# Kernel optimization log

Measured on AMD Instinct MI355X. Metric: run time of the kernel, lower is better.

The kernel has to match this reference:

```python
import jax, jax.numpy as jnp
import numpy as np

D_MODEL = 1024
NUM_HEADS = 16
D_K = D_MODEL // NUM_HEADS
B, S = 2, 2048


def setup_inputs() -> dict:
    key = jax.random.key(0)
    ks = jax.random.split(key, 11)
    scale = 1.0 / np.sqrt(D_MODEL)
    inp = {
        "Q": jax.random.normal(ks[0], (B, S, D_MODEL), jnp.float32),
        "K": jax.random.normal(ks[1], (B, S, D_MODEL), jnp.float32),
        "V": jax.random.normal(ks[2], (B, S, D_MODEL), jnp.float32),
        "mask": jnp.tril(jnp.ones((S, S), jnp.int32))[None, None, :, :],  # causal [1,1,S,S]
        "Wq": jax.random.normal(ks[3], (D_MODEL, D_MODEL), jnp.float32) * scale,
        "bq": jax.random.normal(ks[4], (D_MODEL,), jnp.float32) * scale,
        "Wk": jax.random.normal(ks[5], (D_MODEL, D_MODEL), jnp.float32) * scale,
        "bk": jax.random.normal(ks[6], (D_MODEL,), jnp.float32) * scale,
        "Wv": jax.random.normal(ks[7], (D_MODEL, D_MODEL), jnp.float32) * scale,
        "bv": jax.random.normal(ks[8], (D_MODEL,), jnp.float32) * scale,
        "Wo": jax.random.normal(ks[9], (D_MODEL, D_MODEL), jnp.float32) * scale,
        "bo": jax.random.normal(ks[10], (D_MODEL,), jnp.float32) * scale,
    }
    return inp


def _split_heads(x):
    b, s, _ = x.shape
    return x.reshape(b, s, NUM_HEADS, D_K).transpose(0, 2, 1, 3)  # [B,H,S,d_k]


def reference(Q, K, V, mask, Wq, bq, Wk, bk, Wv, bv, Wo, bo):
    q = _split_heads(Q @ Wq.T + bq)
    k = _split_heads(K @ Wk.T + bk)
    v = _split_heads(V @ Wv.T + bv)
    scores = jnp.einsum("bhqd,bhkd->bhqk", q, k) / jnp.sqrt(jnp.float32(D_K))
    scores = jnp.where(mask == 0, jnp.float32(-1e9), scores)
    probs = jax.nn.softmax(scores, axis=-1)
    attn = jnp.einsum("bhqk,bhkd->bhqd", probs, v)  # [B,H,S,d_k]
    attn = attn.transpose(0, 2, 1, 3).reshape(Q.shape[0], Q.shape[1], D_MODEL)
    return attn @ Wo.T + bo
```

## Files before the change

### kernel.cpp

```cpp
#include <hip/hip_runtime.h>
#include <hip/hip_bf16.h>

typedef __attribute__((ext_vector_type(8))) short short8;
typedef __attribute__((ext_vector_type(4))) short short4v;
typedef __attribute__((ext_vector_type(4))) float f32x4;
typedef __attribute__((ext_vector_type(4))) int i32x4;

static __device__ __forceinline__ short f2bf(float f) {
    __hip_bfloat16 h = __float2bfloat16(f);
    return __builtin_bit_cast(short, h);
}

static __device__ __forceinline__ float exp2fast(float x) {
    float r;
    asm("v_exp_f32 %0, %1" : "=v"(r) : "v"(x));
    return r;
}

static __device__ __forceinline__ unsigned cvt_pk_bf16(float a, float b) {
    unsigned r;
    asm("v_cvt_pk_bf16_f32 %0, %1, %2" : "=v"(r) : "v"(a), "v"(b));
    return r;
}

#define GLOAD16(g, l) __builtin_amdgcn_global_load_lds( \
    (const __attribute__((address_space(1))) void*)(g), \
    (__attribute__((address_space(3))) void*)(l), 16, 0, 0)

__global__ __launch_bounds__(256) void convert_all(
        const float* __restrict__ q, const float* __restrict__ k, const float* __restrict__ v,
        const float* __restrict__ wq, const float* __restrict__ wk,
        const float* __restrict__ wv, const float* __restrict__ wo,
        short* __restrict__ oq, short* __restrict__ ok, short* __restrict__ ov,
        short* __restrict__ owq, short* __restrict__ owk,
        short* __restrict__ owv, short* __restrict__ owo) {
    const int y = blockIdx.y;
    const float* in;
    short* out;
    int n4;
    switch (y) {
        case 0: in = q;  out = oq;  n4 = 1048576; break;
        case 1: in = k;  out = ok;  n4 = 1048576; break;
        case 2: in = v;  out = ov;  n4 = 1048576; break;
        case 3: in = wq; out = owq; n4 = 262144;  break;
        case 4: in = wk; out = owk; n4 = 262144;  break;
        case 5: in = wv; out = owv; n4 = 262144;  break;
        default: in = wo; out = owo; n4 = 262144; break;
    }
    int i = blockIdx.x * blockDim.x + threadIdx.x;
    int stride = gridDim.x * blockDim.x;
    for (; i < n4; i += stride) {
        f32x4 vv = reinterpret_cast<const f32x4*>(in)[i];
        short4v o;
        o.x = f2bf(vv.x); o.y = f2bf(vv.y); o.z = f2bf(vv.z); o.w = f2bf(vv.w);
        reinterpret_cast<short4v*>(out)[i] = o;
    }
}

__global__ __launch_bounds__(256, 3) void gemm_qkv(
        const short* __restrict__ Qb, const short* __restrict__ Kb, const short* __restrict__ Vb,
        const short* __restrict__ Wq, const short* __restrict__ Wk, const short* __restrict__ Wv,
        const float* __restrict__ bq, const float* __restrict__ bk, const float* __restrict__ bv,
        short* __restrict__ q_, short* __restrict__ k_, short* __restrict__ vT) {
    __shared__ __align__(16) short aS[128 * 64];
    __shared__ __align__(16) short bS[128 * 64];
    const int tid = threadIdx.x;
    const int lane = tid & 63;
    const int w = tid >> 6;
    const int wr = w >> 1, wc = w & 1;
    const int l15 = lane & 15, lq = lane >> 4;
    const int lr = lane >> 3;
    const int lcs = ((lane & 7) ^ lr) * 8;
    const int y = blockIdx.y;
    const int wg = (blockIdx.x & 7) * 32 + (blockIdx.x >> 3);
    const int bn = wg & 7;
    const int bm = wg >> 3;

    const short* A = y == 0 ? Qb : y == 1 ? Kb : Vb;
    const short* W = y == 0 ? Wq : y == 1 ? Wk : Wv;
    const float* bias = y == 0 ? bq : y == 1 ? bk : bv;
    const short* Ab = A + (size_t)(bm * 128) * 1024;
    const short* Wb = W + (size_t)(bn * 128) * 1024;

    f32x4 acc[4][4] = {};

    for (int t = 0; t < 16; ++t) {
        const int k0 = t * 64;
#pragma unroll
        for (int j = 0; j < 4; ++j) {
            int r0 = w * 32 + j * 8;
            GLOAD16(&Ab[(size_t)(r0 + lr) * 1024 + k0 + lcs], &aS[r0 * 64]);
        }
#pragma unroll
        for (int j = 0; j < 4; ++j) {
            int r0 = w * 32 + j * 8;
            GLOAD16(&Wb[(size_t)(r0 + lr) * 1024 + k0 + lcs], &bS[r0 * 64]);
        }
        asm volatile("s_waitcnt vmcnt(0)" ::: "memory");
        __builtin_amdgcn_s_barrier();
#pragma unroll
        for (int kf = 0; kf < 2; ++kf) {
            const int ck = ((kf * 4 + lq) ^ (l15 & 7)) * 8;
            short8 af[4], bfr[4];
#pragma unroll
            for (int mi = 0; mi < 4; ++mi)
                af[mi] = *reinterpret_cast<const short8*>(
                    &aS[(wr * 64 + mi * 16 + l15) * 64 + ck]);
#pragma unroll
            for (int ni = 0; ni < 4; ++ni)
                bfr[ni] = *reinterpret_cast<const short8*>(
                    &bS[(wc * 64 + ni * 16 + l15) * 64 + ck]);
#pragma unroll
            for (int mi = 0; mi < 4; ++mi)
#pragma unroll
                for (int ni = 0; ni < 4; ++ni)
                    acc[mi][ni] = __builtin_amdgcn_mfma_f32_16x16x32_bf16(
                        af[mi], bfr[ni], acc[mi][ni], 0, 0, 0);
        }
        asm volatile("s_waitcnt lgkmcnt(0)" ::: "memory");
        __builtin_amdgcn_sched_barrier(0);
        __builtin_amdgcn_s_barrier();
    }

    const float QSCALE = 0.125f * 1.44269504f;
#pragma unroll
    for (int mi = 0; mi < 4; ++mi) {
#pragma unroll
        for (int ni = 0; ni < 4; ++ni) {
#pragma unroll
            for (int i = 0; i < 4; ++i) {
                int m = bm * 128 + wr * 64 + mi * 16 + lq * 4 + i;
                int n = bn * 128 + wc * 64 + ni * 16 + l15;
                float v = acc[mi][ni][i] + bias[n];
                int b = m >> 11, s = m & 2047, h = n >> 6, d = n & 63;
                if (y == 0) {
                    q_[((size_t)(b * 16 + h) * 2048 + s) * 64 + d] = f2bf(v * QSCALE);
                } else if (y == 1) {
                    k_[((size_t)(b * 16 + h) * 2048 + s) * 64 + d] = f2bf(v);
                } else {
                    vT[((size_t)(b * 16 + h) * 64 + d) * 2048 + s] = f2bf(v);
                }
            }
        }
    }
}

__device__ __forceinline__ void gemm_kloop(
        const short* __restrict__ Abase, const short* __restrict__ Wbase,
        short* aSb, short* bSb, f32x4 (&acc)[4][2], int w, int lane) {
    const int lr = lane >> 3;
    const int lcs = ((lane & 7) ^ lr) * 8;
    const int l15 = lane & 15, lq = lane >> 4;
    const int wr = w >> 1, wc = w & 1;
    const int cA0 = ((0 + lq) ^ (l15 & 7)) * 8;
    const int cA1 = ((4 + lq) ^ (l15 & 7)) * 8;

#pragma unroll
    for (int j = 0; j < 4; ++j) {
        int r0 = w * 32 + j * 8;
        GLOAD16(&Abase[(size_t)(r0 + lr) * 1024 + lcs], &aSb[r0 * 64]);
    }
#pragma unroll
    for (int j = 0; j < 2; ++j) {
        int r0 = w * 16 + j * 8;
        GLOAD16(&Wbase[(size_t)(r0 + lr) * 1024 + lcs], &bSb[r0 * 64]);
    }

    for (int t = 0; t < 16; ++t) {
        const int cur = t & 1;
        if (t < 15) {
            const int k0 = (t + 1) * 64;
            const int nb = cur ^ 1;
#pragma unroll
            for (int j = 0; j < 4; ++j) {
                int r0 = w * 32 + j * 8;
                GLOAD16(&Abase[(size_t)(r0 + lr) * 1024 + k0 + lcs], &aSb[nb * 8192 + r0 * 64]);
            }
#pragma unroll
            for (int j = 0; j < 2; ++j) {
                int r0 = w * 16 + j * 8;
                GLOAD16(&Wbase[(size_t)(r0 + lr) * 1024 + k0 + lcs], &bSb[nb * 4096 + r0 * 64]);
            }
            asm volatile("s_waitcnt vmcnt(6)" ::: "memory");
        } else {
            asm volatile("s_waitcnt vmcnt(0)" ::: "memory");
        }
        __builtin_amdgcn_s_barrier();
        __builtin_amdgcn_sched_barrier(0);
#pragma unroll
        for (int kf = 0; kf < 2; ++kf) {
            const int ck = kf ? cA1 : cA0;
            short8 af[4], bfr[2];
#pragma unroll
            for (int mi = 0; mi < 4; ++mi)
                af[mi] = *reinterpret_cast<const short8*>(
                    &aSb[cur * 8192 + (wr * 64 + mi * 16 + l15) * 64 + ck]);
#pragma unroll
            for (int ni = 0; ni < 2; ++ni)
                bfr[ni] = *reinterpret_cast<const short8*>(
                    &bSb[cur * 4096 + (wc * 32 + ni * 16 + l15) * 64 + ck]);
#pragma unroll
            for (int mi = 0; mi < 4; ++mi)
#pragma unroll
                for (int ni = 0; ni < 2; ++ni)
                    acc[mi][ni] = __builtin_amdgcn_mfma_f32_16x16x32_bf16(
                        af[mi], bfr[ni], acc[mi][ni], 0, 0, 0);
        }
        asm volatile("s_waitcnt lgkmcnt(0)" ::: "memory");
        __builtin_amdgcn_sched_barrier(0);
        __builtin_amdgcn_s_barrier();
    }
}

__global__ __launch_bounds__(256, 3) void gemm_o(
        const short* __restrict__ A, const short* __restrict__ W,
        const float* __restrict__ bias, float* __restrict__ out) {
    __shared__ __align__(16) short aSb[2 * 128 * 64];
    __shared__ __align__(16) short bSb[2 * 64 * 64];
    const int tid = threadIdx.x;
    const int lane = tid & 63;
    const int w = tid >> 6;
    const int wg = (blockIdx.x & 7) * 64 + (blockIdx.x >> 3);
    const int bn = wg & 15;
    const int bm = wg >> 4;
    const int l15 = lane & 15, lq = lane >> 4;
    const int wr = w >> 1, wc = w & 1;

    f32x4 acc[4][2] = {};
    gemm_kloop(&A[(size_t)(bm * 128) * 1024], &W[(size_t)(bn * 64) * 1024],
               aSb, bSb, acc, w, lane);

#pragma unroll
    for (int mi = 0; mi < 4; ++mi)
#pragma unroll
        for (int ni = 0; ni < 2; ++ni)
#pragma unroll
            for (int i = 0; i < 4; ++i) {
                int m = bm * 128 + wr * 64 + mi * 16 + lq * 4 + i;
                int n = bn * 64 + wc * 32 + ni * 16 + l15;
                out[(size_t)m * 1024 + n] = acc[mi][ni][i] + bias[n];
            }
}

__global__ __launch_bounds__(256, 4) void attn_fwd(
        const short* __restrict__ qh, const short* __restrict__ kh,
        const short* __restrict__ vT, short* __restrict__ attn) {
    __shared__ __align__(16) short kS[64 * 64];
    __shared__ __align__(16) short vS[64 * 64];
    const int tid = threadIdx.x;
    const int lane = tid & 63;
    const int l15 = lane & 15, lq = lane >> 4;
    const int w = tid >> 6;
    const int hi = (lane >> 5) & 1;
    const int bh = blockIdx.x & 31;
    const int qt = 31 - (blockIdx.x >> 5);
    const int b = bh >> 4, h = bh & 15;
    const size_t head = (size_t)bh * 2048 * 64;
    const short* qp = qh + head;
    const short* kp = kh + head;
    const short* vp = vT + head;
    const int qw0 = qt * 64 + w * 16;

    short8 qf_[2];
#pragma unroll
    for (int kf = 0; kf < 2; ++kf)
        qf_[kf] = *reinterpret_cast<const short8*>(
            &qp[(size_t)(qw0 + l15) * 64 + kf * 32 + lq * 8]);

    f32x4 o[4] = {};
    float m_ = -1e30f, l_ = 0.f;

    const int sr = tid >> 3;
    const int sc8 = tid & 7;
    const int scg = sc8 * 8;
    const int sls = sr * 64 + (sc8 ^ (sr & 7)) * 8;
    const int sls2 = (sr + 32) * 64 + (sc8 ^ (sr & 7)) * 8;

    const int nt = qt + 1;
    short8 kra = *reinterpret_cast<const short8*>(&kp[(size_t)sr * 64 + scg]);
    short8 krb = *reinterpret_cast<const short8*>(&kp[(size_t)(sr + 32) * 64 + scg]);
    short8 vra = *reinterpret_cast<const short8*>(&vp[(size_t)sr * 2048 + scg]);
    short8 vrb = *reinterpret_cast<const short8*>(&vp[(size_t)(sr + 32) * 2048 + scg]);
    *reinterpret_cast<short8*>(&kS[sls]) = kra;
    *reinterpret_cast<short8*>(&kS[sls2]) = krb;
    *reinterpret_cast<short8*>(&vS[sls]) = vra;
    *reinterpret_cast<short8*>(&vS[sls2]) = vrb;
    __syncthreads();

    for (int t = 0; t < nt; ++t) {
        if (t + 1 < nt) {
            kra = *reinterpret_cast<const short8*>(
                &kp[(size_t)((t + 1) * 64 + sr) * 64 + scg]);
            krb = *reinterpret_cast<const short8*>(
                &kp[(size_t)((t + 1) * 64 + sr + 32) * 64 + scg]);
            vra = *reinterpret_cast<const short8*>(
                &vp[(size_t)sr * 2048 + (t + 1) * 64 + scg]);
            vrb = *reinterpret_cast<const short8*>(
                &vp[(size_t)(sr + 32) * 2048 + (t + 1) * 64 + scg]);
        }
        f32x4 s[4] = {};
#pragma unroll
        for (int kf = 0; kf < 2; ++kf) {
            short8 kfr[4];
#pragma unroll
            for (int cf = 0; cf < 4; ++cf)
                kfr[cf] = *reinterpret_cast<const short8*>(
                    &kS[(cf * 16 + l15) * 64 + ((kf * 4 + lq) ^ (l15 & 7)) * 8]);
#pragma unroll
            for (int cf = 0; cf < 4; ++cf)
                s[cf] = __builtin_amdgcn_mfma_f32_16x16x32_bf16(
                    kfr[cf], qf_[kf], s[cf], 0, 0, 0);
        }
        if (t == qt) {
            const int q = qw0 + l15;
#pragma unroll
            for (int cf = 0; cf < 4; ++cf)
#pragma unroll
                for (int i = 0; i < 4; ++i)
                    if (t * 64 + cf * 16 + lq * 4 + i > q) s[cf][i] = -1e30f;
        }
        float pmax = fmaxf(fmaxf(fmaxf(s[0][0], s[0][1]), fmaxf(s[0][2], s[0][3])),
                           fmaxf(fmaxf(s[1][0], s[1][1]), fmaxf(s[1][2], s[1][3])));
        pmax = fmaxf(pmax, fmaxf(fmaxf(fmaxf(s[2][0], s[2][1]), fmaxf(s[2][2], s[2][3])),
                                 fmaxf(fmaxf(s[3][0], s[3][1]), fmaxf(s[3][2], s[3][3]))));
        pmax = fmaxf(pmax, __shfl_xor(pmax, 16));
        pmax = fmaxf(pmax, __shfl_xor(pmax, 32));
        if (!__all(pmax - m_ <= 8.0f)) {
            float mnew = fmaxf(m_, pmax);
            float scl = exp2fast(m_ - mnew);
            m_ = mnew;
            l_ *= scl;
            float s0 = __shfl(scl, lq * 4 + 0);
            float s1 = __shfl(scl, lq * 4 + 1);
            float s2 = __shfl(scl, lq * 4 + 2);
            float s3 = __shfl(scl, lq * 4 + 3);
#pragma unroll
            for (int df = 0; df < 4; ++df) {
                o[df][0] *= s0; o[df][1] *= s1; o[df][2] *= s2; o[df][3] *= s3;
            }
        }
        float rsum = 0.f;
        unsigned P8[8];
#pragma unroll
        for (int cf = 0; cf < 4; ++cf) {
            float p0 = exp2fast(s[cf][0] - m_);
            float p1 = exp2fast(s[cf][1] - m_);
            float p2 = exp2fast(s[cf][2] - m_);
            float p3 = exp2fast(s[cf][3] - m_);
            rsum += (p0 + p1) + (p2 + p3);
            P8[2 * cf]     = cvt_pk_bf16(p0, p1);
            P8[2 * cf + 1] = cvt_pk_bf16(p2, p3);
        }
        rsum += __shfl_xor(rsum, 16);
        rsum += __shfl_xor(rsum, 32);
        l_ += rsum;
#pragma unroll
        for (int kk = 0; kk < 2; ++kk) {
            int dw[4];
#pragma unroll
            for (int j = 0; j < 4; ++j) {
                int src = l15 + 16 * (2 * (lq & 1) + (j >> 1));
                int vlo = __shfl((int)P8[4 * kk + (j & 1)], src);
                int vhi = __shfl((int)P8[4 * kk + 2 + (j & 1)], src);
                dw[j] = hi ? vhi : vlo;
            }
            i32x4 dwv; dwv.x = dw[0]; dwv.y = dw[1]; dwv.z = dw[2]; dwv.w = dw[3];
            short8 pa = __builtin_bit_cast(short8, dwv);
            short8 vb[4];
#pragma unroll
            for (int df = 0; df < 4; ++df)
                vb[df] = *reinterpret_cast<const short8*>(
                    &vS[(df * 16 + l15) * 64 + ((kk * 4 + lq) ^ (l15 & 7)) * 8]);
#pragma unroll
            for (int df = 0; df < 4; ++df)
                o[df] = __builtin_amdgcn_mfma_f32_16x16x32_bf16(
                    pa, vb[df], o[df], 0, 0, 0);
        }
        __syncthreads();
        if (t + 1 < nt) {
            *reinterpret_cast<short8*>(&kS[sls]) = kra;
            *reinterpret_cast<short8*>(&kS[sls2]) = krb;
            *reinterpret_cast<short8*>(&vS[sls]) = vra;
            *reinterpret_cast<short8*>(&vS[sls2]) = vrb;
        }
        __syncthreads();
    }

#pragma unroll
    for (int i = 0; i < 4; ++i) {
        float li = __shfl(l_, lq * 4 + i);
        float rinv = 1.0f / li;
        int sg = qw0 + lq * 4 + i;
        size_t mrow = (size_t)b * 2048 + sg;
#pragma unroll
        for (int df = 0; df < 4; ++df) {
            int col = h * 64 + df * 16 + l15;
            attn[mrow * 1024 + col] = f2bf(o[df][i] * rinv);
        }
    }
}

extern "C" void kernel_launch(void* const* d_in, const int* in_sizes, int n_in,
                              void* d_out, int out_size, void* d_ws, size_t ws_size,
                              hipStream_t stream) {
    const float* Q  = (const float*)d_in[0];
    const float* K  = (const float*)d_in[1];
    const float* V  = (const float*)d_in[2];
    const float* Wq = (const float*)d_in[4];
    const float* bq = (const float*)d_in[5];
    const float* Wk = (const float*)d_in[6];
    const float* bk = (const float*)d_in[7];
    const float* Wv = (const float*)d_in[8];
    const float* bv = (const float*)d_in[9];
    const float* Wo = (const float*)d_in[10];
    const float* bo = (const float*)d_in[11];

    char* ws = (char*)d_ws;
    short* Qb   = (short*)(ws);
    short* Kb   = (short*)(ws + 8388608);
    short* Vb   = (short*)(ws + 16777216);
    short* Wqb  = (short*)(ws + 25165824);
    short* Wkb  = (short*)(ws + 27262976);
    short* Wvb  = (short*)(ws + 29360128);
    short* Wob  = (short*)(ws + 31457280);
    short* q_   = (short*)(ws + 33554432);
    short* k_   = (short*)(ws + 41943040);
    short* vT   = (short*)(ws + 50331648);
    short* attn = Qb;

    dim3 cb(256);
    convert_all<<<dim3(512, 7), cb, 0, stream>>>(Q, K, V, Wq, Wk, Wv, Wo,
                                                 Qb, Kb, Vb, Wqb, Wkb, Wvb, Wob);

    gemm_qkv<<<dim3(256, 3), cb, 0, stream>>>(Qb, Kb, Vb, Wqb, Wkb, Wvb,
                                              bq, bk, bv, q_, k_, vT);

    attn_fwd<<<dim3(1024), cb, 0, stream>>>(q_, k_, vT, attn);

    gemm_o<<<dim3(512), cb, 0, stream>>>(attn, Wob, bo, (float*)d_out);
}
```

Before: 222.1 us.

## Pair causal q-tiles per block, stage vT stores via LDS, retile output GEMM

The attention kernel now gives each block two query tiles (p and 31-p), so causal work is balanced and each K/V tile loaded into LDS serves both tiles. The grid shrinks to 512 blocks and the occupancy hint drops to 2. The V projection epilogue transposes through LDS so it can write 16-byte coalesced stores to vT instead of scattered 2-byte ones. The output GEMM moves to 128x128 tiles with a single-buffered k-loop and 256 blocks. That gives fewer blocks per CU and loses the global-load prefetch overlap the old double-buffered loop had.

```diff
diff --git a/kernel.cpp b/kernel.cpp
--- a/kernel.cpp
+++ b/kernel.cpp
@@ -62,8 +62,9 @@
         const short* __restrict__ Wq, const short* __restrict__ Wk, const short* __restrict__ Wv,
         const float* __restrict__ bq, const float* __restrict__ bk, const float* __restrict__ bv,
         short* __restrict__ q_, short* __restrict__ k_, short* __restrict__ vT) {
-    __shared__ __align__(16) short aS[128 * 64];
-    __shared__ __align__(16) short bS[128 * 64];
+    __shared__ __align__(16) short lds[2 * 128 * 64];
+    short* aS = lds;
+    short* bS = lds + 8192;
     const int tid = threadIdx.x;
     const int lane = tid & 63;
     const int w = tid >> 6;
@@ -123,126 +124,129 @@
     }
 
     const float QSCALE = 0.125f * 1.44269504f;
-#pragma unroll
-    for (int mi = 0; mi < 4; ++mi) {
-#pragma unroll
-        for (int ni = 0; ni < 4; ++ni) {
+    if (y < 2) {
+#pragma unroll
+        for (int mi = 0; mi < 4; ++mi) {
+#pragma unroll
+            for (int ni = 0; ni < 4; ++ni) {
+#pragma unroll
+                for (int i = 0; i < 4; ++i) {
+                    int m = bm * 128 + wr * 64 + mi * 16 + lq * 4 + i;
+                    int n = bn * 128 + wc * 64 + ni * 16 + l15;
+                    float v = acc[mi][ni][i] + bias[n];
+                    int b = m >> 11, s = m & 2047, h = n >> 6, d = n & 63;
+                    if (y == 0)
+                        q_[((size_t)(b * 16 + h) * 2048 + s) * 64 + d] = f2bf(v * QSCALE);
+                    else
+                        k_[((size_t)(b * 16 + h) * 2048 + s) * 64 + d] = f2bf(v);
+                }
+            }
+        }
+    } else {
+#pragma unroll
+        for (int mi = 0; mi < 4; ++mi) {
+#pragma unroll
+            for (int ni = 0; ni < 4; ++ni) {
+                int nl = wc * 64 + ni * 16 + l15;
+                int cc = wr * 8 + mi * 2 + (lq >> 1);
+                int addr = nl * 128 + ((cc ^ (nl & 15)) * 8) + (lq & 1) * 4;
+                short4v pk;
+                pk.x = f2bf(acc[mi][ni][0] + bias[bn * 128 + nl]);
+                pk.y = f2bf(acc[mi][ni][1] + bias[bn * 128 + nl]);
+                pk.z = f2bf(acc[mi][ni][2] + bias[bn * 128 + nl]);
+                pk.w = f2bf(acc[mi][ni][3] + bias[bn * 128 + nl]);
+                *reinterpret_cast<short4v*>(&lds[addr]) = pk;
+            }
+        }
+        __syncthreads();
+        const int bb = bm >> 4;
+        const int s0base = (bm & 15) * 128;
+#pragma unroll
+        for (int j = 0; j < 8; ++j) {
+            int rr = w * 32 + (j & 1) * 16 + (lane >> 2);
+            int cc2 = (j >> 1) * 4 + (lane & 3);
+            short8 val = *reinterpret_cast<const short8*>(
+                &lds[rr * 128 + ((cc2 ^ (rr & 15)) * 8)]);
+            int n = bn * 128 + rr;
+            int hh = n >> 6, d = n & 63;
+            *reinterpret_cast<short8*>(
+                &vT[((size_t)(bb * 16 + hh) * 64 + d) * 2048 + s0base + cc2 * 8]) = val;
+        }
+    }
+}
+
+__global__ __launch_bounds__(256, 3) void gemm_o(
+        const short* __restrict__ A, const short* __restrict__ W,
+        const float* __restrict__ bias, float* __restrict__ out) {
+    __shared__ __align__(16) short lds[2 * 128 * 64];
+    short* aS = lds;
+    short* bS = lds + 8192;
+    const int tid = threadIdx.x;
+    const int lane = tid & 63;
+    const int w = tid >> 6;
+    const int wr = w >> 1, wc = w & 1;
+    const int l15 = lane & 15, lq = lane >> 4;
+    const int lr = lane >> 3;
+    const int lcs = ((lane & 7) ^ lr) * 8;
+    const int wg = (blockIdx.x & 7) * 32 + (blockIdx.x >> 3);
+    const int bn = wg & 7;
+    const int bm = wg >> 3;
+    const short* Ab = A + (size_t)(bm * 128) * 1024;
+    const short* Wb = W + (size_t)(bn * 128) * 1024;
+
+    f32x4 acc[4][4] = {};
+
+    for (int t = 0; t < 16; ++t) {
+        const int k0 = t * 64;
+#pragma unroll
+        for (int j = 0; j < 4; ++j) {
+            int r0 = w * 32 + j * 8;
+            GLOAD16(&Ab[(size_t)(r0 + lr) * 1024 + k0 + lcs], &aS[r0 * 64]);
+        }
+#pragma unroll
+        for (int j = 0; j < 4; ++j) {
+            int r0 = w * 32 + j * 8;
+            GLOAD16(&Wb[(size_t)(r0 + lr) * 1024 + k0 + lcs], &bS[r0 * 64]);
+        }
+        asm volatile("s_waitcnt vmcnt(0)" ::: "memory");
+        __builtin_amdgcn_s_barrier();
+#pragma unroll
+        for (int kf = 0; kf < 2; ++kf) {
+            const int ck = ((kf * 4 + lq) ^ (l15 & 7)) * 8;
+            short8 af[4], bfr[4];
+#pragma unroll
+            for (int mi = 0; mi < 4; ++mi)
+                af[mi] = *reinterpret_cast<const short8*>(
+                    &aS[(wr * 64 + mi * 16 + l15) * 64 + ck]);
+#pragma unroll
+            for (int ni = 0; ni < 4; ++ni)
+                bfr[ni] = *reinterpret_cast<const short8*>(
+                    &bS[(wc * 64 + ni * 16 + l15) * 64 + ck]);
+#pragma unroll
+            for (int mi = 0; mi < 4; ++mi)
+#pragma unroll
+                for (int ni = 0; ni < 4; ++ni)
+                    acc[mi][ni] = __builtin_amdgcn_mfma_f32_16x16x32_bf16(
+                        af[mi], bfr[ni], acc[mi][ni], 0, 0, 0);
+        }
+        asm volatile("s_waitcnt lgkmcnt(0)" ::: "memory");
+        __builtin_amdgcn_sched_barrier(0);
+        __builtin_amdgcn_s_barrier();
+    }
+
+#pragma unroll
+    for (int mi = 0; mi < 4; ++mi)
+#pragma unroll
+        for (int ni = 0; ni < 4; ++ni)
 #pragma unroll
             for (int i = 0; i < 4; ++i) {
                 int m = bm * 128 + wr * 64 + mi * 16 + lq * 4 + i;
                 int n = bn * 128 + wc * 64 + ni * 16 + l15;
-                float v = acc[mi][ni][i] + bias[n];
-                int b = m >> 11, s = m & 2047, h = n >> 6, d = n & 63;
-                if (y == 0) {
-                    q_[((size_t)(b * 16 + h) * 2048 + s) * 64 + d] = f2bf(v * QSCALE);
-                } else if (y == 1) {
-                    k_[((size_t)(b * 16 + h) * 2048 + s) * 64 + d] = f2bf(v);
-                } else {
-                    vT[((size_t)(b * 16 + h) * 64 + d) * 2048 + s] = f2bf(v);
-                }
-            }
-        }
-    }
-}
-
-__device__ __forceinline__ void gemm_kloop(
-        const short* __restrict__ Abase, const short* __restrict__ Wbase,
-        short* aSb, short* bSb, f32x4 (&acc)[4][2], int w, int lane) {
-    const int lr = lane >> 3;
-    const int lcs = ((lane & 7) ^ lr) * 8;
-    const int l15 = lane & 15, lq = lane >> 4;
-    const int wr = w >> 1, wc = w & 1;
-    const int cA0 = ((0 + lq) ^ (l15 & 7)) * 8;
-    const int cA1 = ((4 + lq) ^ (l15 & 7)) * 8;
-
-#pragma unroll
-    for (int j = 0; j < 4; ++j) {
-        int r0 = w * 32 + j * 8;
-        GLOAD16(&Abase[(size_t)(r0 + lr) * 1024 + lcs], &aSb[r0 * 64]);
-    }
-#pragma unroll
-    for (int j = 0; j < 2; ++j) {
-        int r0 = w * 16 + j * 8;
-        GLOAD16(&Wbase[(size_t)(r0 + lr) * 1024 + lcs], &bSb[r0 * 64]);
-    }
-
-    for (int t = 0; t < 16; ++t) {
-        const int cur = t & 1;
-        if (t < 15) {
-            const int k0 = (t + 1) * 64;
-            const int nb = cur ^ 1;
-#pragma unroll
-            for (int j = 0; j < 4; ++j) {
-                int r0 = w * 32 + j * 8;
-                GLOAD16(&Abase[(size_t)(r0 + lr) * 1024 + k0 + lcs], &aSb[nb * 8192 + r0 * 64]);
-            }
-#pragma unroll
-            for (int j = 0; j < 2; ++j) {
-                int r0 = w * 16 + j * 8;
-                GLOAD16(&Wbase[(size_t)(r0 + lr) * 1024 + k0 + lcs], &bSb[nb * 4096 + r0 * 64]);
-            }
-            asm volatile("s_waitcnt vmcnt(6)" ::: "memory");
-        } else {
-            asm volatile("s_waitcnt vmcnt(0)" ::: "memory");
-        }
-        __builtin_amdgcn_s_barrier();
-        __builtin_amdgcn_sched_barrier(0);
-#pragma unroll
-        for (int kf = 0; kf < 2; ++kf) {
-            const int ck = kf ? cA1 : cA0;
-            short8 af[4], bfr[2];
-#pragma unroll
-            for (int mi = 0; mi < 4; ++mi)
-                af[mi] = *reinterpret_cast<const short8*>(
-                    &aSb[cur * 8192 + (wr * 64 + mi * 16 + l15) * 64 + ck]);
-#pragma unroll
-            for (int ni = 0; ni < 2; ++ni)
-                bfr[ni] = *reinterpret_cast<const short8*>(
-                    &bSb[cur * 4096 + (wc * 32 + ni * 16 + l15) * 64 + ck]);
-#pragma unroll
-            for (int mi = 0; mi < 4; ++mi)
-#pragma unroll
-                for (int ni = 0; ni < 2; ++ni)
-                    acc[mi][ni] = __builtin_amdgcn_mfma_f32_16x16x32_bf16(
-                        af[mi], bfr[ni], acc[mi][ni], 0, 0, 0);
-        }
-        asm volatile("s_waitcnt lgkmcnt(0)" ::: "memory");
-        __builtin_amdgcn_sched_barrier(0);
-        __builtin_amdgcn_s_barrier();
-    }
-}
-
-__global__ __launch_bounds__(256, 3) void gemm_o(
-        const short* __restrict__ A, const short* __restrict__ W,
-        const float* __restrict__ bias, float* __restrict__ out) {
-    __shared__ __align__(16) short aSb[2 * 128 * 64];
-    __shared__ __align__(16) short bSb[2 * 64 * 64];
-    const int tid = threadIdx.x;
-    const int lane = tid & 63;
-    const int w = tid >> 6;
-    const int wg = (blockIdx.x & 7) * 64 + (blockIdx.x >> 3);
-    const int bn = wg & 15;
-    const int bm = wg >> 4;
-    const int l15 = lane & 15, lq = lane >> 4;
-    const int wr = w >> 1, wc = w & 1;
-
-    f32x4 acc[4][2] = {};
-    gemm_kloop(&A[(size_t)(bm * 128) * 1024], &W[(size_t)(bn * 64) * 1024],
-               aSb, bSb, acc, w, lane);
-
-#pragma unroll
-    for (int mi = 0; mi < 4; ++mi)
-#pragma unroll
-        for (int ni = 0; ni < 2; ++ni)
-#pragma unroll
-            for (int i = 0; i < 4; ++i) {
-                int m = bm * 128 + wr * 64 + mi * 16 + lq * 4 + i;
-                int n = bn * 64 + wc * 32 + ni * 16 + l15;
                 out[(size_t)m * 1024 + n] = acc[mi][ni][i] + bias[n];
             }
 }
 
-__global__ __launch_bounds__(256, 4) void attn_fwd(
+__global__ __launch_bounds__(256, 2) void attn_fwd(
         const short* __restrict__ qh, const short* __restrict__ kh,
         const short* __restrict__ vT, short* __restrict__ attn) {
     __shared__ __align__(16) short kS[64 * 64];
@@ -253,22 +257,27 @@
     const int w = tid >> 6;
     const int hi = (lane >> 5) & 1;
     const int bh = blockIdx.x & 31;
-    const int qt = 31 - (blockIdx.x >> 5);
+    const int p = blockIdx.x >> 5;
+    const int qtL = p, qtH = 31 - p;
     const int b = bh >> 4, h = bh & 15;
     const size_t head = (size_t)bh * 2048 * 64;
     const short* qp = qh + head;
     const short* kp = kh + head;
     const short* vp = vT + head;
-    const int qw0 = qt * 64 + w * 16;
-
-    short8 qf_[2];
-#pragma unroll
-    for (int kf = 0; kf < 2; ++kf)
-        qf_[kf] = *reinterpret_cast<const short8*>(
-            &qp[(size_t)(qw0 + l15) * 64 + kf * 32 + lq * 8]);
-
-    f32x4 o[4] = {};
-    float m_ = -1e30f, l_ = 0.f;
+    const int qL0 = qtL * 64 + w * 16;
+    const int qH0 = qtH * 64 + w * 16;
+
+    short8 qfL_[2], qfH_[2];
+#pragma unroll
+    for (int kf = 0; kf < 2; ++kf) {
+        qfL_[kf] = *reinterpret_cast<const short8*>(
+            &qp[(size_t)(qL0 + l15) * 64 + kf * 32 + lq * 8]);
+        qfH_[kf] = *reinterpret_cast<const short8*>(
+            &qp[(size_t)(qH0 + l15) * 64 + kf * 32 + lq * 8]);
+    }
+
+    f32x4 oH[4] = {}, oL[4] = {};
+    float mH = -1e30f, lH = 0.f, mL = -1e30f, lL = 0.f;
 
     const int sr = tid >> 3;
     const int sc8 = tid & 7;
@@ -276,49 +285,8 @@
     const int sls = sr * 64 + (sc8 ^ (sr & 7)) * 8;
     const int sls2 = (sr + 32) * 64 + (sc8 ^ (sr & 7)) * 8;
 
-    const int nt = qt + 1;
-    short8 kra = *reinterpret_cast<const short8*>(&kp[(size_t)sr * 64 + scg]);
-    short8 krb = *reinterpret_cast<const short8*>(&kp[(size_t)(sr + 32) * 64 + scg]);
-    short8 vra = *reinterpret_cast<const short8*>(&vp[(size_t)sr * 2048 + scg]);
-    short8 vrb = *reinterpret_cast<const short8*>(&vp[(size_t)(sr + 32) * 2048 + scg]);
-    *reinterpret_cast<short8*>(&kS[sls]) = kra;
-    *reinterpret_cast<short8*>(&kS[sls2]) = krb;
-    *reinterpret_cast<short8*>(&vS[sls]) = vra;
-    *reinterpret_cast<short8*>(&vS[sls2]) = vrb;
-    __syncthreads();
-
-    for (int t = 0; t < nt; ++t) {
-        if (t + 1 < nt) {
-            kra = *reinterpret_cast<const short8*>(
-                &kp[(size_t)((t + 1) * 64 + sr) * 64 + scg]);
-            krb = *reinterpret_cast<const short8*>(
-                &kp[(size_t)((t + 1) * 64 + sr + 32) * 64 + scg]);
-            vra = *reinterpret_cast<const short8*>(
-                &vp[(size_t)sr * 2048 + (t + 1) * 64 + scg]);
-            vrb = *reinterpret_cast<const short8*>(
-                &vp[(size_t)(sr + 32) * 2048 + (t + 1) * 64 + scg]);
-        }
-        f32x4 s[4] = {};
-#pragma unroll
-        for (int kf = 0; kf < 2; ++kf) {
-            short8 kfr[4];
-#pragma unroll
-            for (int cf = 0; cf < 4; ++cf)
-                kfr[cf] = *reinterpret_cast<const short8*>(
-                    &kS[(cf * 16 + l15) * 64 + ((kf * 4 + lq) ^ (l15 & 7)) * 8]);
-#pragma unroll
-            for (int cf = 0; cf < 4; ++cf)
-                s[cf] = __builtin_amdgcn_mfma_f32_16x16x32_bf16(
-                    kfr[cf], qf_[kf], s[cf], 0, 0, 0);
-        }
-        if (t == qt) {
-            const int q = qw0 + l15;
-#pragma unroll
-            for (int cf = 0; cf < 4; ++cf)
-#pragma unroll
-                for (int i = 0; i < 4; ++i)
-                    if (t * 64 + cf * 16 + lq * 4 + i > q) s[cf][i] = -1e30f;
-        }
+    auto softmax = [&](f32x4 (&s)[4], float& m_, float& l_, f32x4 (&o)[4],
+                       unsigned (&P8)[8]) {
         float pmax = fmaxf(fmaxf(fmaxf(s[0][0], s[0][1]), fmaxf(s[0][2], s[0][3])),
                            fmaxf(fmaxf(s[1][0], s[1][1]), fmaxf(s[1][2], s[1][3])));
         pmax = fmaxf(pmax, fmaxf(fmaxf(fmaxf(s[2][0], s[2][1]), fmaxf(s[2][2], s[2][3])),
@@ -340,7 +308,6 @@
             }
         }
         float rsum = 0.f;
-        unsigned P8[8];
 #pragma unroll
         for (int cf = 0; cf < 4; ++cf) {
             float p0 = exp2fast(s[cf][0] - m_);
@@ -354,27 +321,108 @@
         rsum += __shfl_xor(rsum, 16);
         rsum += __shfl_xor(rsum, 32);
         l_ += rsum;
+    };
+
+    const int nt = qtH + 1;
+    short8 kra = *reinterpret_cast<const short8*>(&kp[(size_t)sr * 64 + scg]);
+    short8 krb = *reinterpret_cast<const short8*>(&kp[(size_t)(sr + 32) * 64 + scg]);
+    short8 vra = *reinterpret_cast<const short8*>(&vp[(size_t)sr * 2048 + scg]);
+    short8 vrb = *reinterpret_cast<const short8*>(&vp[(size_t)(sr + 32) * 2048 + scg]);
+    *reinterpret_cast<short8*>(&kS[sls]) = kra;
+    *reinterpret_cast<short8*>(&kS[sls2]) = krb;
+    *reinterpret_cast<short8*>(&vS[sls]) = vra;
+    *reinterpret_cast<short8*>(&vS[sls2]) = vrb;
+    __syncthreads();
+
+    for (int t = 0; t < nt; ++t) {
+        if (t + 1 < nt) {
+            kra = *reinterpret_cast<const short8*>(
+                &kp[(size_t)((t + 1) * 64 + sr) * 64 + scg]);
+            krb = *reinterpret_cast<const short8*>(
+                &kp[(size_t)((t + 1) * 64 + sr + 32) * 64 + scg]);
+            vra = *reinterpret_cast<const short8*>(
+                &vp[(size_t)sr * 2048 + (t + 1) * 64 + scg]);
+            vrb = *reinterpret_cast<const short8*>(
+                &vp[(size_t)(sr + 32) * 2048 + (t + 1) * 64 + scg]);
+        }
+        const bool la = (t <= qtL);
+        f32x4 sH[4] = {}, sL[4] = {};
+#pragma unroll
+        for (int kf = 0; kf < 2; ++kf) {
+            short8 kfr[4];
+#pragma unroll
+            for (int cf = 0; cf < 4; ++cf)
+                kfr[cf] = *reinterpret_cast<const short8*>(
+                    &kS[(cf * 16 + l15) * 64 + ((kf * 4 + lq) ^ (l15 & 7)) * 8]);
+#pragma unroll
+            for (int cf = 0; cf < 4; ++cf)
+                sH[cf] = __builtin_amdgcn_mfma_f32_16x16x32_bf16(
+                    kfr[cf], qfH_[kf], sH[cf], 0, 0, 0);
+            if (la) {
+#pragma unroll
+                for (int cf = 0; cf < 4; ++cf)
+                    sL[cf] = __builtin_amdgcn_mfma_f32_16x16x32_bf16(
+                        kfr[cf], qfL_[kf], sL[cf], 0, 0, 0);
+            }
+        }
+        if (t == qtH) {
+            const int q = qH0 + l15;
+#pragma unroll
+            for (int cf = 0; cf < 4; ++cf)
+#pragma unroll
+                for (int i = 0; i < 4; ++i)
+                    if (t * 64 + cf * 16 + lq * 4 + i > q) sH[cf][i] = -1e30f;
+        }
+        if (la && t == qtL) {
+            const int q = qL0 + l15;
+#pragma unroll
+            for (int cf = 0; cf < 4; ++cf)
+#pragma unroll
+                for (int i = 0; i < 4; ++i)
+                    if (t * 64 + cf * 16 + lq * 4 + i > q) sL[cf][i] = -1e30f;
+        }
+        unsigned P8H[8], P8L[8];
+        softmax(sH, mH, lH, oH, P8H);
+        if (la) softmax(sL, mL, lL, oL, P8L);
 #pragma unroll
         for (int kk = 0; kk < 2; ++kk) {
-            int dw[4];
-#pragma unroll
-            for (int j = 0; j < 4; ++j) {
-                int src = l15 + 16 * (2 * (lq & 1) + (j >> 1));
-                int vlo = __shfl((int)P8[4 * kk + (j & 1)], src);
-                int vhi = __shfl((int)P8[4 * kk + 2 + (j & 1)], src);
-                dw[j] = hi ? vhi : vlo;
-            }
-            i32x4 dwv; dwv.x = dw[0]; dwv.y = dw[1]; dwv.z = dw[2]; dwv.w = dw[3];
-            short8 pa = __builtin_bit_cast(short8, dwv);
             short8 vb[4];
 #pragma unroll
             for (int df = 0; df < 4; ++df)
                 vb[df] = *reinterpret_cast<const short8*>(
                     &vS[(df * 16 + l15) * 64 + ((kk * 4 + lq) ^ (l15 & 7)) * 8]);
-#pragma unroll
-            for (int df = 0; df < 4; ++df)
-                o[df] = __builtin_amdgcn_mfma_f32_16x16x32_bf16(
-                    pa, vb[df], o[df], 0, 0, 0);
+            {
+                int dw[4];
+#pragma unroll
+                for (int j = 0; j < 4; ++j) {
+                    int src = l15 + 16 * (2 * (lq & 1) + (j >> 1));
+                    int vlo = __shfl((int)P8H[4 * kk + (j & 1)], src);
+                    int vhi = __shfl((int)P8H[4 * kk + 2 + (j & 1)], src);
+                    dw[j] = hi ? vhi : vlo;
+                }
+                i32x4 dwv; dwv.x = dw[0]; dwv.y = dw[1]; dwv.z = dw[2]; dwv.w = dw[3];
+                short8 pa = __builtin_bit_cast(short8, dwv);
+#pragma unroll
+                for (int df = 0; df < 4; ++df)
+                    oH[df] = __builtin_amdgcn_mfma_f32_16x16x32_bf16(
+                        pa, vb[df], oH[df], 0, 0, 0);
+            }
+            if (la) {
+                int dw[4];
+#pragma unroll
+                for (int j = 0; j < 4; ++j) {
+                    int src = l15 + 16 * (2 * (lq & 1) + (j >> 1));
+                    int vlo = __shfl((int)P8L[4 * kk + (j & 1)], src);
+                    int vhi = __shfl((int)P8L[4 * kk + 2 + (j & 1)], src);
+                    dw[j] = hi ? vhi : vlo;
+                }
+                i32x4 dwv; dwv.x = dw[0]; dwv.y = dw[1]; dwv.z = dw[2]; dwv.w = dw[3];
+                short8 pa = __builtin_bit_cast(short8, dwv);
+#pragma unroll
+                for (int df = 0; df < 4; ++df)
+                    oL[df] = __builtin_amdgcn_mfma_f32_16x16x32_bf16(
+                        pa, vb[df], oL[df], 0, 0, 0);
+            }
         }
         __syncthreads();
         if (t + 1 < nt) {
@@ -388,14 +436,19 @@
 
 #pragma unroll
     for (int i = 0; i < 4; ++i) {
-        float li = __shfl(l_, lq * 4 + i);
-        float rinv = 1.0f / li;
-        int sg = qw0 + lq * 4 + i;
-        size_t mrow = (size_t)b * 2048 + sg;
+        float liH = __shfl(lH, lq * 4 + i);
+        float liL = __shfl(lL, lq * 4 + i);
+        float rH = 1.0f / liH;
+        float rL = 1.0f / liL;
+        int sgH = qH0 + lq * 4 + i;
+        int sgL = qL0 + lq * 4 + i;
+        size_t mrH = (size_t)b * 2048 + sgH;
+        size_t mrL = (size_t)b * 2048 + sgL;
 #pragma unroll
         for (int df = 0; df < 4; ++df) {
             int col = h * 64 + df * 16 + l15;
-            attn[mrow * 1024 + col] = f2bf(o[df][i] * rinv);
+            attn[mrH * 1024 + col] = f2bf(oH[df][i] * rH);
+            attn[mrL * 1024 + col] = f2bf(oL[df][i] * rL);
         }
     }
 }
@@ -435,7 +488,7 @@
     gemm_qkv<<<dim3(256, 3), cb, 0, stream>>>(Qb, Kb, Vb, Wqb, Wkb, Wvb,
                                               bq, bk, bv, q_, k_, vT);
 
-    attn_fwd<<<dim3(1024), cb, 0, stream>>>(q_, k_, vT, attn);
-
-    gemm_o<<<dim3(512), cb, 0, stream>>>(attn, Wob, bo, (float*)d_out);
-}
+    attn_fwd<<<dim3(512), cb, 0, stream>>>(q_, k_, vT, attn);
+
+    gemm_o<<<dim3(256), cb, 0, stream>>>(attn, Wob, bo, (float*)d_out);
+}
```

Result: slower. 227.6 us (+2.5%).
